# Kernel tuning notes

Measured on AMD Instinct MI355X. Metric: run time of the kernel, lower is better.

The kernel has to match this reference:

```python
import jax, jax.numpy as jnp
import numpy as np

B, T, C = 4, 2048, 1024
H = 16
D = C // H  # head_dim = 64


def setup_inputs() -> dict:
    key = jax.random.key(0)
    k1, k2, k3 = jax.random.split(key, 3)
    x = jax.random.normal(k1, (B, T, C), dtype=jnp.float32)
    # torch Linear weights are [out_features, in_features]; scale like default init
    W_qkv = jax.random.normal(k2, (3 * C, C), dtype=jnp.float32) * (1.0 / np.sqrt(C))
    W_proj = jax.random.normal(k3, (C, C), dtype=jnp.float32) * (1.0 / np.sqrt(C))
    return {"x": x, "W_qkv": W_qkv, "W_proj": W_proj}


def reference(x, W_qkv, W_proj):
    # qkv projection: x @ W_qkv.T -> (B,T,3C), split into q,k,v
    qkv = jnp.einsum('btc,oc->bto', x, W_qkv)
    q, k, v = jnp.split(qkv, 3, axis=-1)
    # reshape to (B,H,T,D)
    q = q.reshape(B, T, H, D).transpose(0, 2, 1, 3)
    k = k.reshape(B, T, H, D).transpose(0, 2, 1, 3)
    v = v.reshape(B, T, H, D).transpose(0, 2, 1, 3)
    scale = jnp.sqrt(jnp.float32(D))
    # explicit (B,H,T,T) scores, as in the original module
    attn = jnp.einsum('bhqd,bhkd->bhqk', q, k) / scale
    causal = jnp.tril(jnp.ones((T, T), dtype=bool))
    attn = jnp.where(causal, attn, -jnp.inf)
    attn = jax.nn.softmax(attn, axis=-1)
    out = jnp.einsum('bhqk,bhkd->bhqd', attn, v)
    out = out.transpose(0, 2, 1, 3).reshape(B, T, C)
    return jnp.einsum('btc,oc->bto', out, W_proj)
```

## Files before the change

### kernel.cpp

```cpp
#include <hip/hip_runtime.h>

typedef __attribute__((ext_vector_type(8))) short short8;
typedef __attribute__((ext_vector_type(4))) float f32x4;
typedef __attribute__((ext_vector_type(16))) float f32x16;
typedef __attribute__((ext_vector_type(4))) unsigned int u32x4;

#define AS1(p) ((const __attribute__((address_space(1))) void*)(p))
#define AS3(p) ((__attribute__((address_space(3))) void*)(p))

#define B_ 4
#define T_ 2048
#define C_ 1024
#define H_ 16
#define D_ 64
#define M_ (B_*T_)

#define MFIX 16.0f

__device__ __forceinline__ unsigned short f2bf(float f) {
  union { float f; unsigned u; } v; v.f = f;
  return (unsigned short)((v.u + 0x7fffu + ((v.u >> 16) & 1u)) >> 16);
}

__device__ __forceinline__ unsigned cvt_pk_bf16(float lo, float hi2) {
  unsigned r;
  asm("v_cvt_pk_bf16_f32 %0, %1, %2" : "=v"(r) : "v"(lo), "v"(hi2));
  return r;
}

__device__ __forceinline__ float exp2_fast(float x) {
  return __builtin_amdgcn_exp2f(x);
}

__global__ void cast_all(const float* __restrict__ x, const float* __restrict__ wq,
                         const float* __restrict__ wp,
                         unsigned short* __restrict__ xb, unsigned short* __restrict__ wqb,
                         unsigned short* __restrict__ wpb) {
  const int n0 = M_ * C_;
  const int n1 = 3 * C_ * C_;
  const int n2 = C_ * C_;
  const int ntot = n0 + n1 + n2;
  int i = (blockIdx.x * blockDim.x + threadIdx.x) * 4;
  int stride = gridDim.x * blockDim.x * 4;
  for (; i < ntot; i += stride) {
    const float* src; unsigned short* dst; int off;
    if (i < n0)            { src = x;  dst = xb;  off = i; }
    else if (i < n0 + n1)  { src = wq; dst = wqb; off = i - n0; }
    else                   { src = wp; dst = wpb; off = i - n0 - n1; }
    float4 f = *reinterpret_cast<const float4*>(src + off);
    ushort4 o;
    o.x = f2bf(f.x); o.y = f2bf(f.y); o.z = f2bf(f.z); o.w = f2bf(f.w);
    *reinterpret_cast<ushort4*>(dst + off) = o;
  }
}

template<int EPI>
__global__ __launch_bounds__(256) void gemm_bt(
    const unsigned short* __restrict__ A, const unsigned short* __restrict__ Bt,
    float* __restrict__ Cout, int M, int N, int K,
    unsigned short* __restrict__ qb, unsigned short* __restrict__ kb,
    unsigned short* __restrict__ vtb) {
  __shared__ unsigned short SMEM[2][2][128 * 32];
  const int tid = threadIdx.x;
  const int lane = tid & 63;
  const int w = tid >> 6;
  const int wr = w >> 1, wc = w & 1;
  const int lr = lane & 15, lg = lane >> 4;
  const int ntiles = N >> 7;
  const int nwg = gridDim.x;
  const int cpx = nwg >> 3;
  const int wg = (blockIdx.x & 7) * cpx + (blockIdx.x >> 3);
  const int mt = wg / ntiles, nt = wg % ntiles;
  const int m0 = mt << 7, n0 = nt << 7;

  f32x4 acc[4][4];
  #pragma unroll
  for (int i = 0; i < 4; i++)
    #pragma unroll
    for (int j = 0; j < 4; j++) acc[i][j] = (f32x4){0.f, 0.f, 0.f, 0.f};

  const int wbase = tid & ~63;

  auto stage = [&](int buf, int k0) {
    #pragma unroll
    for (int t = 0; t < 2; t++) {
      int slot = t * 256 + tid;
      int row = slot >> 2, kg = slot & 3;
      const unsigned short* ga = A + (size_t)(m0 + row) * K + k0 + kg * 8;
      char* la = (char*)&SMEM[0][buf][0] + (size_t)(t * 256 + wbase) * 16;
      __builtin_amdgcn_global_load_lds(AS1(ga), AS3(la), 16, 0, 0);
      const unsigned short* gb = Bt + (size_t)(n0 + row) * K + k0 + kg * 8;
      char* lb = (char*)&SMEM[1][buf][0] + (size_t)(t * 256 + wbase) * 16;
      __builtin_amdgcn_global_load_lds(AS1(gb), AS3(lb), 16, 0, 0);
    }
  };

  const int nIter = K >> 5;
  stage(0, 0);
  __syncthreads();

  for (int it = 0; it < nIter; ++it) {
    const int cur = it & 1;
    if (it + 1 < nIter) stage(cur ^ 1, (it + 1) << 5);

    short8 af[4], bf[4];
    #pragma unroll
    for (int i = 0; i < 4; i++) {
      af[i] = *reinterpret_cast<const short8*>(&SMEM[0][cur][(wr * 64 + i * 16 + lr) * 32 + lg * 8]);
      bf[i] = *reinterpret_cast<const short8*>(&SMEM[1][cur][(wc * 64 + i * 16 + lr) * 32 + lg * 8]);
    }
    #pragma unroll
    for (int i = 0; i < 4; i++)
      #pragma unroll
      for (int j = 0; j < 4; j++)
        acc[i][j] = __builtin_amdgcn_mfma_f32_16x16x32_bf16(af[i], bf[j], acc[i][j], 0, 0, 0);

    __syncthreads();
  }

  if (EPI == 1 && n0 >= 2 * C_) {
    unsigned short* vt = &SMEM[0][0][0];
    #pragma unroll
    for (int i = 0; i < 4; i++) {
      #pragma unroll
      for (int j = 0; j < 4; j++) {
        int rl = wr * 64 + i * 16 + lg * 4;
        int cl = wc * 64 + j * 16 + lr;
        int rsw = rl ^ ((cl & 7) << 3);
        short4 pk;
        pk.x = (short)f2bf(acc[i][j][0]); pk.y = (short)f2bf(acc[i][j][1]);
        pk.z = (short)f2bf(acc[i][j][2]); pk.w = (short)f2bf(acc[i][j][3]);
        *reinterpret_cast<short4*>(vt + cl * 128 + rsw) = pk;
      }
    }
    __syncthreads();
    const int cl = tid >> 1;
    const int rbase = (tid & 1) * 64;
    const int c = (n0 + cl) & 1023;
    const int h2 = c >> 6, d2 = c & 63;
    const int b2 = m0 >> 11;
    const int t2b = (m0 & 2047) + rbase;
    unsigned short* dst = vtb + (((size_t)(b2 * H_ + h2)) * D_ + d2) * T_ + t2b;
    #pragma unroll
    for (int u = 0; u < 8; u++) {
      int rl = rbase + u * 8;
      int rsw = rl ^ ((cl & 7) << 3);
      *reinterpret_cast<short8*>(dst + u * 8) =
          *reinterpret_cast<const short8*>(vt + cl * 128 + rsw);
    }
  } else {
    #pragma unroll
    for (int i = 0; i < 4; i++) {
      #pragma unroll
      for (int j = 0; j < 4; j++) {
        #pragma unroll
        for (int r = 0; r < 4; r++) {
          int row = m0 + wr * 64 + i * 16 + lg * 4 + r;
          int col = n0 + wc * 64 + j * 16 + lr;
          float v = acc[i][j][r];
          if (EPI == 0) {
            Cout[(size_t)row * N + col] = v;
          } else {
            int which = col >> 10;
            int c = col & 1023;
            int h = c >> 6, d = c & 63;
            int b = row >> 11, t2 = row & 2047;
            if (which == 0) {
              qb[(((size_t)(b * H_ + h)) * T_ + t2) * D_ + d] = f2bf(v * 0.18033688f);
            } else {
              kb[(((size_t)(b * H_ + h)) * T_ + t2) * D_ + d] = f2bf(v);
            }
          }
        }
      }
    }
  }
}

__global__ __launch_bounds__(64, 1) void attn_fwd(
    const unsigned short* __restrict__ qb, const unsigned short* __restrict__ kb,
    const unsigned short* __restrict__ vtb, unsigned short* __restrict__ ob) {
  __shared__ unsigned short Kl[2 * 64 * 64];
  const int lane = threadIdx.x;
  const int q31 = lane & 31;
  const int hi = lane >> 5;

  const int bid = blockIdx.x;
  const int bh = (bid & 7) * 8 + ((bid >> 3) & 7);
  const int qt = 31 - (bid >> 6);
  const int qb0 = qt << 6;
  const int b = bh >> 4, h = bh & 15;

  const unsigned short* Q  = qb  + (size_t)bh * T_ * D_;
  const unsigned short* Kp = kb  + (size_t)bh * T_ * D_;
  const unsigned short* Vt = vtb + (size_t)bh * D_ * T_;

  const int qgA = qb0 + q31;
  const int qgB = qb0 + 32 + q31;

  short8 qfA[4], qfB[4];
  #pragma unroll
  for (int ch = 0; ch < 4; ch++) {
    qfA[ch] = *reinterpret_cast<const short8*>(Q + qgA * D_ + ch * 16 + hi * 8);
    qfB[ch] = *reinterpret_cast<const short8*>(Q + qgB * D_ + ch * 16 + hi * 8);
  }

  f32x16 accA0, accA1, accB0, accB1;
  #pragma unroll
  for (int r = 0; r < 16; r++) { accA0[r] = 0.f; accA1[r] = 0.f; accB0[r] = 0.f; accB1[r] = 0.f; }
  float lA = 0.f, lB = 0.f;

  auto stage = [&](int buf, int k0) {
    #pragma unroll
    for (int sh = 0; sh < 8; sh++) {
      int s = sh * 64 + lane;
      int row = s >> 3;
      int src = ((s & 7) * 16) ^ ((row & 7) << 4);
      const unsigned short* g = Kp + (k0 + row) * D_ + (src >> 1);
      char* l = (char*)Kl + buf * 8192 + sh * 1024;
      __builtin_amdgcn_global_load_lds(AS1(g), AS3(l), 16, 0, 0);
    }
  };

  const int nt = qt + 1;
  stage(0, 0);

  for (int t = 0; t < nt; t++) {
    const int k0 = t * 64;
    if (t + 1 < nt) {
      stage((t + 1) & 1, k0 + 64);
      asm volatile("s_waitcnt vmcnt(8)" ::: "memory");
    } else {
      asm volatile("s_waitcnt vmcnt(0)" ::: "memory");
    }
    __builtin_amdgcn_sched_barrier(0);

    short8 vf[2][4];
    #pragma unroll
    for (int ds = 0; ds < 2; ds++)
      #pragma unroll
      for (int kk = 0; kk < 4; kk++)
        vf[ds][kk] = *reinterpret_cast<const short8*>(
            Vt + (ds * 32 + q31) * T_ + k0 + kk * 16 + hi * 8);
    __builtin_amdgcn_sched_barrier(0);

    const char* kbase = (const char*)Kl + (t & 1) * 8192;

    f32x16 sA0, sA1, sB0, sB1;
    #pragma unroll
    for (int r = 0; r < 16; r++) { sA0[r] = 0.f; sA1[r] = 0.f; sB0[r] = 0.f; sB1[r] = 0.f; }
    __builtin_amdgcn_s_setprio(1);
    #pragma unroll
    for (int kc = 0; kc < 2; kc++) {
      const int row = kc * 32 + q31;
      const int sw = (row & 7) << 4;
      #pragma unroll
      for (int ch = 0; ch < 4; ch++) {
        short8 kf = *reinterpret_cast<const short8*>(kbase + row * 128 + ((ch * 32 + hi * 16) ^ sw));
        if (kc == 0) {
          sA0 = __builtin_amdgcn_mfma_f32_32x32x16_bf16(kf, qfA[ch], sA0, 0, 0, 0);
          sB0 = __builtin_amdgcn_mfma_f32_32x32x16_bf16(kf, qfB[ch], sB0, 0, 0, 0);
        } else {
          sA1 = __builtin_amdgcn_mfma_f32_32x32x16_bf16(kf, qfA[ch], sA1, 0, 0, 0);
          sB1 = __builtin_amdgcn_mfma_f32_32x32x16_bf16(kf, qfB[ch], sB1, 0, 0, 0);
        }
      }
    }
    __builtin_amdgcn_s_setprio(0);

    if (t == nt - 1) {
      #pragma unroll
      for (int r = 0; r < 16; r++) {
        const int kl = (r & 3) + 8 * (r >> 2) + 4 * hi;
        if (k0 + kl > qgA)      sA0[r] = -INFINITY;
        if (k0 + 32 + kl > qgA) sA1[r] = -INFINITY;
        if (k0 + kl > qgB)      sB0[r] = -INFINITY;
        if (k0 + 32 + kl > qgB) sB1[r] = -INFINITY;
      }
    }

    #pragma unroll
    for (int r = 0; r < 16; r++) {
      sA0[r] = exp2_fast(sA0[r] - MFIX); sA1[r] = exp2_fast(sA1[r] - MFIX);
      sB0[r] = exp2_fast(sB0[r] - MFIX); sB1[r] = exp2_fast(sB1[r] - MFIX);
    }
    {
      float tsA[8], tsB[8];
      #pragma unroll
      for (int r = 0; r < 8; r++) {
        tsA[r] = (sA0[r] + sA0[r + 8]) + (sA1[r] + sA1[r + 8]);
        tsB[r] = (sB0[r] + sB0[r + 8]) + (sB1[r] + sB1[r + 8]);
      }
      #pragma unroll
      for (int off = 4; off > 0; off >>= 1)
        #pragma unroll
        for (int r = 0; r < off; r++) { tsA[r] += tsA[r + off]; tsB[r] += tsB[r + off]; }
      lA += tsA[0];
      lB += tsB[0];
    }

    #pragma unroll
    for (int kc = 0; kc < 2; kc++) {
      unsigned w8A[8], rw8A[8], w8B[8], rw8B[8];
      #pragma unroll
      for (int j = 0; j < 8; j++) {
        float aA  = (kc == 0) ? sA0[2 * j] : sA1[2 * j];
        float bA  = (kc == 0) ? sA0[2 * j + 1] : sA1[2 * j + 1];
        w8A[j] = cvt_pk_bf16(aA, bA);
        float aB  = (kc == 0) ? sB0[2 * j] : sB1[2 * j];
        float bB  = (kc == 0) ? sB0[2 * j + 1] : sB1[2 * j + 1];
        w8B[j] = cvt_pk_bf16(aB, bB);
      }
      #pragma unroll
      for (int j = 0; j < 8; j++) {
        rw8A[j] = (unsigned)__shfl_xor((int)w8A[j], 32);
        rw8B[j] = (unsigned)__shfl_xor((int)w8B[j], 32);
      }

      __builtin_amdgcn_s_setprio(1);
      #pragma unroll
      for (int ks = 0; ks < 2; ks++) {
        unsigned a0 = hi ? rw8A[4 * ks + 2] : w8A[4 * ks + 0];
        unsigned a1 = hi ? rw8A[4 * ks + 3] : w8A[4 * ks + 1];
        unsigned a2 = hi ? w8A[4 * ks + 2]  : rw8A[4 * ks + 0];
        unsigned a3 = hi ? w8A[4 * ks + 3]  : rw8A[4 * ks + 1];
        u32x4 pwA = {a0, a1, a2, a3};
        unsigned b0 = hi ? rw8B[4 * ks + 2] : w8B[4 * ks + 0];
        unsigned b1 = hi ? rw8B[4 * ks + 3] : w8B[4 * ks + 1];
        unsigned b2 = hi ? w8B[4 * ks + 2]  : rw8B[4 * ks + 0];
        unsigned b3 = hi ? w8B[4 * ks + 3]  : rw8B[4 * ks + 1];
        u32x4 pwB = {b0, b1, b2, b3};
        union { u32x4 u; short8 s; } cvA, cvB;
        cvA.u = pwA; cvB.u = pwB;
        const int kk = kc * 2 + ks;
        #pragma unroll
        for (int ds = 0; ds < 2; ds++) {
          if (ds == 0) {
            accA0 = __builtin_amdgcn_mfma_f32_32x32x16_bf16(vf[0][kk], cvA.s, accA0, 0, 0, 0);
            accB0 = __builtin_amdgcn_mfma_f32_32x32x16_bf16(vf[0][kk], cvB.s, accB0, 0, 0, 0);
          } else {
            accA1 = __builtin_amdgcn_mfma_f32_32x32x16_bf16(vf[1][kk], cvA.s, accA1, 0, 0, 0);
            accB1 = __builtin_amdgcn_mfma_f32_32x32x16_bf16(vf[1][kk], cvB.s, accB1, 0, 0, 0);
          }
        }
      }
      __builtin_amdgcn_s_setprio(0);
    }
  }

  lA += __shfl_xor(lA, 32);
  lB += __shfl_xor(lB, 32);

  {
    const float invA = 1.f / lA;
    unsigned short* orow = ob + ((size_t)(b * T_ + qgA)) * C_ + h * D_;
    #pragma unroll
    for (int ds = 0; ds < 2; ds++) {
      #pragma unroll
      for (int g = 0; g < 4; g++) {
        ushort4 o4;
        if (ds == 0) {
          o4.x = f2bf(accA0[4 * g + 0] * invA); o4.y = f2bf(accA0[4 * g + 1] * invA);
          o4.z = f2bf(accA0[4 * g + 2] * invA); o4.w = f2bf(accA0[4 * g + 3] * invA);
        } else {
          o4.x = f2bf(accA1[4 * g + 0] * invA); o4.y = f2bf(accA1[4 * g + 1] * invA);
          o4.z = f2bf(accA1[4 * g + 2] * invA); o4.w = f2bf(accA1[4 * g + 3] * invA);
        }
        *reinterpret_cast<ushort4*>(orow + ds * 32 + 8 * g + 4 * hi) = o4;
      }
    }
  }
  {
    const float invB = 1.f / lB;
    unsigned short* orow = ob + ((size_t)(b * T_ + qgB)) * C_ + h * D_;
    #pragma unroll
    for (int ds = 0; ds < 2; ds++) {
      #pragma unroll
      for (int g = 0; g < 4; g++) {
        ushort4 o4;
        if (ds == 0) {
          o4.x = f2bf(accB0[4 * g + 0] * invB); o4.y = f2bf(accB0[4 * g + 1] * invB);
          o4.z = f2bf(accB0[4 * g + 2] * invB); o4.w = f2bf(accB0[4 * g + 3] * invB);
        } else {
          o4.x = f2bf(accB1[4 * g + 0] * invB); o4.y = f2bf(accB1[4 * g + 1] * invB);
          o4.z = f2bf(accB1[4 * g + 2] * invB); o4.w = f2bf(accB1[4 * g + 3] * invB);
        }
        *reinterpret_cast<ushort4*>(orow + ds * 32 + 8 * g + 4 * hi) = o4;
      }
    }
  }
}

extern "C" void kernel_launch(void* const* d_in, const int* in_sizes, int n_in,
                              void* d_out, int out_size, void* d_ws, size_t ws_size,
                              hipStream_t stream) {
  const float* x = (const float*)d_in[0];
  const float* W_qkv = (const float*)d_in[1];
  const float* W_proj = (const float*)d_in[2];
  float* out = (float*)d_out;

  char* ws = (char*)d_ws;
  unsigned short* xb     = (unsigned short*)(ws);
  unsigned short* wqkvb  = (unsigned short*)(ws + 16777216);
  unsigned short* wprojb = (unsigned short*)(ws + 23068672);
  unsigned short* qb     = (unsigned short*)(ws + 25165824);
  unsigned short* kb     = (unsigned short*)(ws + 41943040);
  unsigned short* vtb    = (unsigned short*)(ws + 58720256);
  unsigned short* ob     = xb;

  cast_all<<<2048, 256, 0, stream>>>(x, W_qkv, W_proj, xb, wqkvb, wprojb);

  gemm_bt<1><<<(M_ / 128) * (3 * C_ / 128), 256, 0, stream>>>(
      xb, wqkvb, nullptr, M_, 3 * C_, C_, qb, kb, vtb);

  attn_fwd<<<B_ * H_ * (T_ / 64), 64, 0, stream>>>(qb, kb, vtb, ob);

  gemm_bt<0><<<(M_ / 128) * (C_ / 128), 256, 0, stream>>>(
      ob, wprojb, out, M_, C_, C_, nullptr, nullptr, nullptr);
}
```

Measured before the change: 193.1 us.

## Split causal KV loop across two waves per attention block and merge via LDS

Attention blocks now run two wavefronts, each processing half of the key/value tiles for the same 64 query rows with its own double-buffered LDS K staging. Afterwards the second wave writes its partial output accumulators and row sums to shared memory, and the first wave adds them and writes the normalized result. This relies on the fixed softmax max offset so partials add directly. It aims to increase latency hiding and per-CU parallelism, at the cost of doubled LDS use, a sync, and a serial merge step.

```diff
diff --git a/kernel.cpp b/kernel.cpp
--- a/kernel.cpp
+++ b/kernel.cpp
@@ -177,11 +177,14 @@
   }
 }
 
-__global__ __launch_bounds__(64, 1) void attn_fwd(
+__global__ __launch_bounds__(128, 1) void attn_fwd(
     const unsigned short* __restrict__ qb, const unsigned short* __restrict__ kb,
     const unsigned short* __restrict__ vtb, unsigned short* __restrict__ ob) {
-  __shared__ unsigned short Kl[2 * 64 * 64];
-  const int lane = threadIdx.x;
+  __shared__ unsigned short Kl[2][2][64 * 64];
+  __shared__ float lbuf[128];
+  const int tid = threadIdx.x;
+  const int lane = tid & 63;
+  const int w = tid >> 6;
   const int q31 = lane & 31;
   const int hi = lane >> 5;
 
@@ -217,18 +220,23 @@
       int row = s >> 3;
       int src = ((s & 7) * 16) ^ ((row & 7) << 4);
       const unsigned short* g = Kp + (k0 + row) * D_ + (src >> 1);
-      char* l = (char*)Kl + buf * 8192 + sh * 1024;
+      char* l = (char*)&Kl[w][buf][0] + sh * 1024;
       __builtin_amdgcn_global_load_lds(AS1(g), AS3(l), 16, 0, 0);
     }
   };
 
   const int nt = qt + 1;
-  stage(0, 0);
-
-  for (int t = 0; t < nt; t++) {
+  const int half = nt >> 1;
+  const int tstart = (w == 0) ? 0 : half;
+  const int tend   = (w == 0) ? half : nt;
+
+  if (tstart < tend) stage(0, tstart * 64);
+
+  for (int t = tstart; t < tend; t++) {
     const int k0 = t * 64;
-    if (t + 1 < nt) {
-      stage((t + 1) & 1, k0 + 64);
+    const int buf = (t - tstart) & 1;
+    if (t + 1 < tend) {
+      stage(buf ^ 1, k0 + 64);
       asm volatile("s_waitcnt vmcnt(8)" ::: "memory");
     } else {
       asm volatile("s_waitcnt vmcnt(0)" ::: "memory");
@@ -244,7 +252,7 @@
             Vt + (ds * 32 + q31) * T_ + k0 + kk * 16 + hi * 8);
     __builtin_amdgcn_sched_barrier(0);
 
-    const char* kbase = (const char*)Kl + (t & 1) * 8192;
+    const char* kbase = (const char*)&Kl[w][buf][0];
 
     f32x16 sA0, sA1, sB0, sB1;
     #pragma unroll
@@ -348,44 +356,69 @@
     }
   }
 
-  lA += __shfl_xor(lA, 32);
-  lB += __shfl_xor(lB, 32);
-
-  {
-    const float invA = 1.f / lA;
-    unsigned short* orow = ob + ((size_t)(b * T_ + qgA)) * C_ + h * D_;
-    #pragma unroll
-    for (int ds = 0; ds < 2; ds++) {
-      #pragma unroll
-      for (int g = 0; g < 4; g++) {
-        ushort4 o4;
-        if (ds == 0) {
-          o4.x = f2bf(accA0[4 * g + 0] * invA); o4.y = f2bf(accA0[4 * g + 1] * invA);
-          o4.z = f2bf(accA0[4 * g + 2] * invA); o4.w = f2bf(accA0[4 * g + 3] * invA);
-        } else {
-          o4.x = f2bf(accA1[4 * g + 0] * invA); o4.y = f2bf(accA1[4 * g + 1] * invA);
-          o4.z = f2bf(accA1[4 * g + 2] * invA); o4.w = f2bf(accA1[4 * g + 3] * invA);
+  if (w == 1) {
+    float* mbuf = (float*)&Kl[1][0][0];
+    #pragma unroll
+    for (int r = 0; r < 16; r++) {
+      mbuf[(r)      * 64 + lane] = accA0[r];
+      mbuf[(16 + r) * 64 + lane] = accA1[r];
+      mbuf[(32 + r) * 64 + lane] = accB0[r];
+      mbuf[(48 + r) * 64 + lane] = accB1[r];
+    }
+    lbuf[lane] = lA;
+    lbuf[64 + lane] = lB;
+  }
+  __syncthreads();
+  if (w == 0) {
+    const float* mbuf = (const float*)&Kl[1][0][0];
+    #pragma unroll
+    for (int r = 0; r < 16; r++) {
+      accA0[r] += mbuf[(r)      * 64 + lane];
+      accA1[r] += mbuf[(16 + r) * 64 + lane];
+      accB0[r] += mbuf[(32 + r) * 64 + lane];
+      accB1[r] += mbuf[(48 + r) * 64 + lane];
+    }
+    lA += lbuf[lane];
+    lB += lbuf[64 + lane];
+    lA += __shfl_xor(lA, 32);
+    lB += __shfl_xor(lB, 32);
+
+    {
+      const float invA = 1.f / lA;
+      unsigned short* orow = ob + ((size_t)(b * T_ + qgA)) * C_ + h * D_;
+      #pragma unroll
+      for (int ds = 0; ds < 2; ds++) {
+        #pragma unroll
+        for (int g = 0; g < 4; g++) {
+          ushort4 o4;
+          if (ds == 0) {
+            o4.x = f2bf(accA0[4 * g + 0] * invA); o4.y = f2bf(accA0[4 * g + 1] * invA);
+            o4.z = f2bf(accA0[4 * g + 2] * invA); o4.w = f2bf(accA0[4 * g + 3] * invA);
+          } else {
+            o4.x = f2bf(accA1[4 * g + 0] * invA); o4.y = f2bf(accA1[4 * g + 1] * invA);
+            o4.z = f2bf(accA1[4 * g + 2] * invA); o4.w = f2bf(accA1[4 * g + 3] * invA);
+          }
+          *reinterpret_cast<ushort4*>(orow + ds * 32 + 8 * g + 4 * hi) = o4;
         }
-        *reinterpret_cast<ushort4*>(orow + ds * 32 + 8 * g + 4 * hi) = o4;
-      }
-    }
-  }
-  {
-    const float invB = 1.f / lB;
-    unsigned short* orow = ob + ((size_t)(b * T_ + qgB)) * C_ + h * D_;
-    #pragma unroll
-    for (int ds = 0; ds < 2; ds++) {
-      #pragma unroll
-      for (int g = 0; g < 4; g++) {
-        ushort4 o4;
-        if (ds == 0) {
-          o4.x = f2bf(accB0[4 * g + 0] * invB); o4.y = f2bf(accB0[4 * g + 1] * invB);
-          o4.z = f2bf(accB0[4 * g + 2] * invB); o4.w = f2bf(accB0[4 * g + 3] * invB);
-        } else {
-          o4.x = f2bf(accB1[4 * g + 0] * invB); o4.y = f2bf(accB1[4 * g + 1] * invB);
-          o4.z = f2bf(accB1[4 * g + 2] * invB); o4.w = f2bf(accB1[4 * g + 3] * invB);
+      }
+    }
+    {
+      const float invB = 1.f / lB;
+      unsigned short* orow = ob + ((size_t)(b * T_ + qgB)) * C_ + h * D_;
+      #pragma unroll
+      for (int ds = 0; ds < 2; ds++) {
+        #pragma unroll
+        for (int g = 0; g < 4; g++) {
+          ushort4 o4;
+          if (ds == 0) {
+            o4.x = f2bf(accB0[4 * g + 0] * invB); o4.y = f2bf(accB0[4 * g + 1] * invB);
+            o4.z = f2bf(accB0[4 * g + 2] * invB); o4.w = f2bf(accB0[4 * g + 3] * invB);
+          } else {
+            o4.x = f2bf(accB1[4 * g + 0] * invB); o4.y = f2bf(accB1[4 * g + 1] * invB);
+            o4.z = f2bf(accB1[4 * g + 2] * invB); o4.w = f2bf(accB1[4 * g + 3] * invB);
+          }
+          *reinterpret_cast<ushort4*>(orow + ds * 32 + 8 * g + 4 * hi) = o4;
         }
-        *reinterpret_cast<ushort4*>(orow + ds * 32 + 8 * g + 4 * hi) = o4;
       }
     }
   }
@@ -413,7 +446,7 @@
   gemm_bt<1><<<(M_ / 128) * (3 * C_ / 128), 256, 0, stream>>>(
       xb, wqkvb, nullptr, M_, 3 * C_, C_, qb, kb, vtb);
 
-  attn_fwd<<<B_ * H_ * (T_ / 64), 64, 0, stream>>>(qb, kb, vtb, ob);
+  attn_fwd<<<B_ * H_ * (T_ / 64), 128, 0, stream>>>(qb, kb, vtb, ob);
 
   gemm_bt<0><<<(M_ / 128) * (C_ / 128), 256, 0, stream>>>(
       ob, wprojb, out, M_, C_, C_, nullptr, nullptr, nullptr);
```

Measured after the change: 207.4 us. 1.07x slower.
